# Optimization experiments

Measured on AMD Instinct MI355X. Metric: run time of the kernel, lower is better.

The kernel has to match this reference:

```python
import jax, jax.numpy as jnp
import numpy as np

EPS = 1e-7  # tf.keras.backend.epsilon()
ROUTING = 3
C, L = 32, 32

def squash(s):
    # 'Dynamic routing between capsules' squash: (|s|^2/(1+|s|^2)) * s/|s|
    n = jnp.linalg.norm(s, axis=-1, keepdims=True)
    return (n ** 2 / (1 + n ** 2) / (n + EPS)) * s

def setup_inputs() -> dict:
    key = jax.random.key(0)
    k1, k2 = jax.random.split(key)
    B, H, Wd, iC, iL = 32, 8, 8, 32, 32
    inputs = jax.random.normal(k1, (B, H, Wd, iC, iL), dtype=jnp.float32)
    N = H * Wd * iC  # 2048 input capsules
    # glorot_uniform for W: [N, input_L, C*L]
    limit = float(np.sqrt(6.0 / (iL + C * L)))
    W = jax.random.uniform(k2, (N, iL, C * L), minval=-limit, maxval=limit, dtype=jnp.float32)
    biases = jnp.zeros((C, L), dtype=jnp.float32)  # 'zeros' initializer
    return {"inputs": inputs, "W": W, "biases": biases}

def reference(inputs, W, biases):
    B = inputs.shape[0]
    N, iL = W.shape[0], W.shape[1]
    x = inputs.reshape(B, N, iL)
    # per-capsule prediction: u[b,j,k] = sum_i x[b,j,i] * W[j,i,k]
    u = jnp.einsum('bji,jik->bjk', x, W).reshape(B, N, C, L)
    b = jnp.zeros((B, N, C, 1), dtype=u.dtype)
    v = jnp.zeros((B, C, L), dtype=u.dtype)
    for r in range(ROUTING):
        c = jax.nn.softmax(b, axis=2)                 # coupling coeffs over C
        s = jnp.sum(u * c, axis=1) + biases           # [B,C,L]
        # NOTE: CapsuleAttentionBlock applied here in original (source not
        # provided in this module); treated as identity.
        v = squash(s)                                 # [B,C,L]
        if r < ROUTING - 1:
            b = b + jnp.sum(u * v[:, None, :, :], axis=-1, keepdims=True)
    return v
```

## Files before the change

kernel.cpp:

```cpp
#include <hip/hip_runtime.h>
#include <hip/hip_bf16.h>

#define NB    32
#define NCAP  2048
#define CL    1024
#define ILEN  32

__device__ inline unsigned short f32_to_bf16_rne(float f) {
    unsigned int u = __float_as_uint(f);
    u += 0x7FFFu + ((u >> 16) & 1u);
    return (unsigned short)(u >> 16);
}

__device__ inline void unpack8(uint4 a, float* f) {
    f[0] = __uint_as_float(a.x << 16);
    f[1] = __uint_as_float(a.x & 0xFFFF0000u);
    f[2] = __uint_as_float(a.y << 16);
    f[3] = __uint_as_float(a.y & 0xFFFF0000u);
    f[4] = __uint_as_float(a.z << 16);
    f[5] = __uint_as_float(a.z & 0xFFFF0000u);
    f[6] = __uint_as_float(a.w << 16);
    f[7] = __uint_as_float(a.w & 0xFFFF0000u);
}

__global__ __launch_bounds__(256) void compute_u(const float* __restrict__ x,
                                                 const float* __restrict__ W,
                                                 unsigned short* __restrict__ u) {
    const int j  = blockIdx.x >> 2;
    const int kq = blockIdx.x & 3;
    const int t  = threadIdx.x;

    __shared__ float xs[32 * 32];

    {
        int b  = t >> 3;
        int i4 = (t & 7) << 2;
        float4 v = *(const float4*)(x + ((size_t)b * NCAP + j) * ILEN + i4);
        xs[(i4 + 0) * 32 + b] = v.x;
        xs[(i4 + 1) * 32 + b] = v.y;
        xs[(i4 + 2) * 32 + b] = v.z;
        xs[(i4 + 3) * 32 + b] = v.w;
    }
    __syncthreads();

    const int lane = t & 63;
    const int wv   = t >> 6;

    const float* Wp = W + (size_t)j * (ILEN * CL) + kq * 256 + (lane << 2);

    float acc[8][4];
#pragma unroll
    for (int bb = 0; bb < 8; ++bb)
#pragma unroll
        for (int q = 0; q < 4; ++q) acc[bb][q] = 0.f;

    float4 wbuf[4];
#pragma unroll
    for (int p = 0; p < 4; ++p) wbuf[p] = *(const float4*)(Wp + (size_t)p * CL);

#pragma unroll
    for (int i = 0; i < 32; ++i) {
        float4 w4 = wbuf[i & 3];
        if (i + 4 < 32) wbuf[i & 3] = *(const float4*)(Wp + (size_t)(i + 4) * CL);
        float4 xa = *(const float4*)(xs + i * 32 + wv * 8);
        float4 xb = *(const float4*)(xs + i * 32 + wv * 8 + 4);
        float xv[8] = {xa.x, xa.y, xa.z, xa.w, xb.x, xb.y, xb.z, xb.w};
#pragma unroll
        for (int bb = 0; bb < 8; ++bb) {
            acc[bb][0] += xv[bb] * w4.x;
            acc[bb][1] += xv[bb] * w4.y;
            acc[bb][2] += xv[bb] * w4.z;
            acc[bb][3] += xv[bb] * w4.w;
        }
    }

    const int k = kq * 256 + (lane << 2);
#pragma unroll
    for (int bb = 0; bb < 8; ++bb) {
        int b = wv * 8 + bb;
        ushort4 o;
        o.x = f32_to_bf16_rne(acc[bb][0]);
        o.y = f32_to_bf16_rne(acc[bb][1]);
        o.z = f32_to_bf16_rne(acc[bb][2]);
        o.w = f32_to_bf16_rne(acc[bb][3]);
        *(ushort4*)(u + ((size_t)b * NCAP + j) * CL + k) = o;
    }
}

template<bool HAS_V>
__global__ __launch_bounds__(256) void route_pass(const unsigned short* __restrict__ u,
                                                  const float* __restrict__ vlog,
                                                  float* __restrict__ spart) {
    const int b    = blockIdx.x;
    const int jc   = blockIdx.y;
    const int t    = threadIdx.x;
    const int wv   = t >> 6;
    const int lane = t & 63;
    const int c0   = lane >> 2;
    const int sub  = lane & 3;
    const int e0   = c0 * 32 + sub * 8;

    float vme0[8], vme1[8];
    if (HAS_V) {
        const float* vb = vlog + b * CL;
        *(float4*)(vme0)     = *(const float4*)(vb + e0);
        *(float4*)(vme0 + 4) = *(const float4*)(vb + e0 + 4);
        *(float4*)(vme1)     = *(const float4*)(vb + e0 + 512);
        *(float4*)(vme1 + 4) = *(const float4*)(vb + e0 + 516);
    }

    const int jbase = jc * 64 + wv * 16;
    const unsigned short* ub = u + ((size_t)b * NCAP + jbase) * CL;

    float acc0[8], acc1[8];
#pragma unroll
    for (int e = 0; e < 8; ++e) { acc0[e] = 0.f; acc1[e] = 0.f; }

    uint4 a0 = *(const uint4*)(ub + 0 * CL + e0);
    uint4 g0 = *(const uint4*)(ub + 0 * CL + e0 + 512);
    uint4 a1 = *(const uint4*)(ub + 1 * CL + e0);
    uint4 g1 = *(const uint4*)(ub + 1 * CL + e0 + 512);

    for (int jj = 0; jj < 16; ++jj) {
        int jn = (jj + 2 < 16) ? (jj + 2) : 15;
        uint4 a2 = *(const uint4*)(ub + (size_t)jn * CL + e0);
        uint4 g2 = *(const uint4*)(ub + (size_t)jn * CL + e0 + 512);

        float uf0[8], uf1[8];
        unpack8(a0, uf0);
        unpack8(g0, uf1);

        float cw0, cw1;
        if (HAS_V) {
            float p0 = 0.f, p1 = 0.f;
#pragma unroll
            for (int e = 0; e < 8; ++e) { p0 += uf0[e] * vme0[e]; p1 += uf1[e] * vme1[e]; }
            p0 += __shfl_xor(p0, 1); p0 += __shfl_xor(p0, 2);
            p1 += __shfl_xor(p1, 1); p1 += __shfl_xor(p1, 2);
            float m = fmaxf(p0, p1);
            m = fmaxf(m, __shfl_xor(m, 4));
            m = fmaxf(m, __shfl_xor(m, 8));
            m = fmaxf(m, __shfl_xor(m, 16));
            m = fmaxf(m, __shfl_xor(m, 32));
            float ex0 = __expf(p0 - m);
            float ex1 = __expf(p1 - m);
            float ssum = ex0 + ex1;
            ssum += __shfl_xor(ssum, 4);
            ssum += __shfl_xor(ssum, 8);
            ssum += __shfl_xor(ssum, 16);
            ssum += __shfl_xor(ssum, 32);
            float inv = __builtin_amdgcn_rcpf(ssum);
            cw0 = ex0 * inv;
            cw1 = ex1 * inv;
        } else {
            cw0 = 0.03125f;
            cw1 = 0.03125f;
        }
#pragma unroll
        for (int e = 0; e < 8; ++e) {
            acc0[e] += cw0 * uf0[e];
            acc1[e] += cw1 * uf1[e];
        }
        a0 = a1; g0 = g1; a1 = a2; g1 = g2;
    }

    __shared__ float red[4][1024];
    *(float4*)(&red[wv][e0])       = *(float4*)(acc0);
    *(float4*)(&red[wv][e0 + 4])   = *(float4*)(acc0 + 4);
    *(float4*)(&red[wv][e0 + 512]) = *(float4*)(acc1);
    *(float4*)(&red[wv][e0 + 516]) = *(float4*)(acc1 + 4);
    __syncthreads();

    const int o = t * 4;
    float4 r0 = *(float4*)(&red[0][o]);
    float4 r1 = *(float4*)(&red[1][o]);
    float4 r2 = *(float4*)(&red[2][o]);
    float4 r3 = *(float4*)(&red[3][o]);
    float4 r;
    r.x = (r0.x + r1.x) + (r2.x + r3.x);
    r.y = (r0.y + r1.y) + (r2.y + r3.y);
    r.z = (r0.z + r1.z) + (r2.z + r3.z);
    r.w = (r0.w + r1.w) + (r2.w + r3.w);
    *(float4*)(spart + ((size_t)b * 32 + jc) * CL + o) = r;
}

__global__ __launch_bounds__(256) void squash_kernel(const float* __restrict__ spart,
                                                     const float* __restrict__ biases,
                                                     float* __restrict__ vout,
                                                     float* __restrict__ vlog_out,
                                                     const float* __restrict__ vprev) {
    const int b = blockIdx.x;
    const int t = threadIdx.x;

    float4 sv = make_float4(0.f, 0.f, 0.f, 0.f);
#pragma unroll
    for (int p = 0; p < 32; ++p) {
        float4 q = *(const float4*)(spart + ((size_t)b * 32 + p) * CL + t * 4);
        sv.x += q.x; sv.y += q.y; sv.z += q.z; sv.w += q.w;
    }
    float4 bi = *(const float4*)(biases + t * 4);
    sv.x += bi.x; sv.y += bi.y; sv.z += bi.z; sv.w += bi.w;

    float n2 = sv.x * sv.x + sv.y * sv.y + sv.z * sv.z + sv.w * sv.w;
    n2 += __shfl_xor(n2, 1);
    n2 += __shfl_xor(n2, 2);
    n2 += __shfl_xor(n2, 4);

    float n = sqrtf(n2);
    float f = n2 / ((1.f + n2) * (n + 1e-7f));

    float4 v;
    v.x = f * sv.x; v.y = f * sv.y; v.z = f * sv.z; v.w = f * sv.w;
    *(float4*)(vout + b * CL + t * 4) = v;

    if (vlog_out != nullptr) {
        float4 a = make_float4(0.f, 0.f, 0.f, 0.f);
        if (vprev != nullptr) a = *(const float4*)(vprev + b * CL + t * 4);
        float4 o;
        o.x = v.x + a.x; o.y = v.y + a.y; o.z = v.z + a.z; o.w = v.w + a.w;
        *(float4*)(vlog_out + b * CL + t * 4) = o;
    }
}

extern "C" void kernel_launch(void* const* d_in, const int* in_sizes, int n_in,
                              void* d_out, int out_size, void* d_ws, size_t ws_size,
                              hipStream_t stream) {
    const float* x      = (const float*)d_in[0];
    const float* W      = (const float*)d_in[1];
    const float* biases = (const float*)d_in[2];
    float* out = (float*)d_out;

    unsigned short* u = (unsigned short*)d_ws;
    float* fb    = (float*)((char*)d_ws + (size_t)NB * NCAP * CL * 2);
    float* spart = fb;
    float* v0    = spart + 1048576;
    float* vl2   = v0 + 32768;
    float* vdmp  = vl2 + 32768;

    compute_u<<<NCAP * 4, 256, 0, stream>>>(x, W, u);

    dim3 rg(NB, 32);
    route_pass<false><<<rg, 256, 0, stream>>>(u, nullptr, spart);
    squash_kernel<<<NB, 256, 0, stream>>>(spart, biases, v0, nullptr, nullptr);
    route_pass<true><<<rg, 256, 0, stream>>>(u, v0, spart);
    squash_kernel<<<NB, 256, 0, stream>>>(spart, biases, vdmp, vl2, v0);
    route_pass<true><<<rg, 256, 0, stream>>>(u, vl2, spart);
    squash_kernel<<<NB, 256, 0, stream>>>(spart, biases, out, nullptr, nullptr);
}
```

Before: 468.5 us.

## Fuse first routing pass into prediction kernel via per-tile partial sums

The prediction kernel now handles 16 capsules per block and also accumulates the uniform-coupling first-iteration sum in registers, writing per-tile partial sums. This removes the first full `route_pass` read of the bf16 prediction tensor. The price is a grid that shrinks from 8192 to 512 blocks, which lowers latency hiding on the W stream. It also adds a 16 MB partial buffer that a 32-block squash kernel must reduce over 128 partials.

```diff
diff --git a/kernel.cpp b/kernel.cpp
--- a/kernel.cpp
+++ b/kernel.cpp
@@ -5,6 +5,7 @@
 #define NCAP  2048
 #define CL    1024
 #define ILEN  32
+#define JT    16
 
 __device__ inline unsigned short f32_to_bf16_rne(float f) {
     unsigned int u = __float_as_uint(f);
@@ -23,67 +24,98 @@
     f[7] = __uint_as_float(a.w & 0xFFFF0000u);
 }
 
-__global__ __launch_bounds__(256) void compute_u(const float* __restrict__ x,
-                                                 const float* __restrict__ W,
-                                                 unsigned short* __restrict__ u) {
-    const int j  = blockIdx.x >> 2;
+__global__ __launch_bounds__(256) void compute_u_fused(const float* __restrict__ x,
+                                                       const float* __restrict__ W,
+                                                       unsigned short* __restrict__ u,
+                                                       float* __restrict__ s0part) {
+    const int jt = blockIdx.x >> 2;
     const int kq = blockIdx.x & 3;
+    const int j0 = jt * JT;
     const int t  = threadIdx.x;
 
-    __shared__ float xs[32 * 32];
+    __shared__ float xs[JT][32][32];
 
     {
-        int b  = t >> 3;
-        int i4 = (t & 7) << 2;
-        float4 v = *(const float4*)(x + ((size_t)b * NCAP + j) * ILEN + i4);
-        xs[(i4 + 0) * 32 + b] = v.x;
-        xs[(i4 + 1) * 32 + b] = v.y;
-        xs[(i4 + 2) * 32 + b] = v.z;
-        xs[(i4 + 3) * 32 + b] = v.w;
+        const int b  = t >> 3;
+        const int i4 = (t & 7) << 2;
+#pragma unroll
+        for (int jj = 0; jj < JT; ++jj) {
+            float4 v = *(const float4*)(x + ((size_t)b * NCAP + j0 + jj) * ILEN + i4);
+            xs[jj][i4 + 0][b] = v.x;
+            xs[jj][i4 + 1][b] = v.y;
+            xs[jj][i4 + 2][b] = v.z;
+            xs[jj][i4 + 3][b] = v.w;
+        }
     }
     __syncthreads();
 
     const int lane = t & 63;
     const int wv   = t >> 6;
 
-    const float* Wp = W + (size_t)j * (ILEN * CL) + kq * 256 + (lane << 2);
-
-    float acc[8][4];
+    const float* Wp = W + (size_t)j0 * (ILEN * CL) + kq * 256 + (lane << 2);
+    const int k = kq * 256 + (lane << 2);
+
+    float s0[8][4];
 #pragma unroll
     for (int bb = 0; bb < 8; ++bb)
 #pragma unroll
-        for (int q = 0; q < 4; ++q) acc[bb][q] = 0.f;
-
-    float4 wbuf[4];
-#pragma unroll
-    for (int p = 0; p < 4; ++p) wbuf[p] = *(const float4*)(Wp + (size_t)p * CL);
-
-#pragma unroll
-    for (int i = 0; i < 32; ++i) {
-        float4 w4 = wbuf[i & 3];
-        if (i + 4 < 32) wbuf[i & 3] = *(const float4*)(Wp + (size_t)(i + 4) * CL);
-        float4 xa = *(const float4*)(xs + i * 32 + wv * 8);
-        float4 xb = *(const float4*)(xs + i * 32 + wv * 8 + 4);
-        float xv[8] = {xa.x, xa.y, xa.z, xa.w, xb.x, xb.y, xb.z, xb.w};
+        for (int q = 0; q < 4; ++q) s0[bb][q] = 0.f;
+
+    float4 ring[4];
+#pragma unroll
+    for (int p = 0; p < 4; ++p) ring[p] = *(const float4*)(Wp + (size_t)p * CL);
+
+    for (int jj = 0; jj < JT; ++jj) {
+        float acc[8][4];
+#pragma unroll
+        for (int bb = 0; bb < 8; ++bb)
+#pragma unroll
+            for (int q = 0; q < 4; ++q) acc[bb][q] = 0.f;
+
+#pragma unroll
+        for (int i = 0; i < 32; ++i) {
+            float4 w4 = ring[i & 3];
+            int rn = jj * 32 + i + 4;
+            if (rn > JT * 32 - 1) rn = JT * 32 - 1;
+            ring[i & 3] = *(const float4*)(Wp + (size_t)rn * CL);
+
+            float4 xa = *(const float4*)(&xs[jj][i][wv * 8]);
+            float4 xb = *(const float4*)(&xs[jj][i][wv * 8 + 4]);
+            float xv[8] = {xa.x, xa.y, xa.z, xa.w, xb.x, xb.y, xb.z, xb.w};
+#pragma unroll
+            for (int bb = 0; bb < 8; ++bb) {
+                acc[bb][0] += xv[bb] * w4.x;
+                acc[bb][1] += xv[bb] * w4.y;
+                acc[bb][2] += xv[bb] * w4.z;
+                acc[bb][3] += xv[bb] * w4.w;
+            }
+        }
+
 #pragma unroll
         for (int bb = 0; bb < 8; ++bb) {
-            acc[bb][0] += xv[bb] * w4.x;
-            acc[bb][1] += xv[bb] * w4.y;
-            acc[bb][2] += xv[bb] * w4.z;
-            acc[bb][3] += xv[bb] * w4.w;
-        }
-    }
-
-    const int k = kq * 256 + (lane << 2);
+            const int b = wv * 8 + bb;
+            s0[bb][0] += acc[bb][0];
+            s0[bb][1] += acc[bb][1];
+            s0[bb][2] += acc[bb][2];
+            s0[bb][3] += acc[bb][3];
+            ushort4 o;
+            o.x = f32_to_bf16_rne(acc[bb][0]);
+            o.y = f32_to_bf16_rne(acc[bb][1]);
+            o.z = f32_to_bf16_rne(acc[bb][2]);
+            o.w = f32_to_bf16_rne(acc[bb][3]);
+            *(ushort4*)(u + ((size_t)b * NCAP + j0 + jj) * CL + k) = o;
+        }
+    }
+
 #pragma unroll
     for (int bb = 0; bb < 8; ++bb) {
-        int b = wv * 8 + bb;
-        ushort4 o;
-        o.x = f32_to_bf16_rne(acc[bb][0]);
-        o.y = f32_to_bf16_rne(acc[bb][1]);
-        o.z = f32_to_bf16_rne(acc[bb][2]);
-        o.w = f32_to_bf16_rne(acc[bb][3]);
-        *(ushort4*)(u + ((size_t)b * NCAP + j) * CL + k) = o;
+        const int b = wv * 8 + bb;
+        float4 o;
+        o.x = s0[bb][0] * 0.03125f;
+        o.y = s0[bb][1] * 0.03125f;
+        o.z = s0[bb][2] * 0.03125f;
+        o.w = s0[bb][3] * 0.03125f;
+        *(float4*)(s0part + ((size_t)b * 128 + jt) * CL + k) = o;
     }
 }
 
@@ -184,6 +216,7 @@
     *(float4*)(spart + ((size_t)b * 32 + jc) * CL + o) = r;
 }
 
+template<int P>
 __global__ __launch_bounds__(256) void squash_kernel(const float* __restrict__ spart,
                                                      const float* __restrict__ biases,
                                                      float* __restrict__ vout,
@@ -193,9 +226,9 @@
     const int t = threadIdx.x;
 
     float4 sv = make_float4(0.f, 0.f, 0.f, 0.f);
-#pragma unroll
-    for (int p = 0; p < 32; ++p) {
-        float4 q = *(const float4*)(spart + ((size_t)b * 32 + p) * CL + t * 4);
+#pragma unroll 8
+    for (int p = 0; p < P; ++p) {
+        float4 q = *(const float4*)(spart + ((size_t)b * P + p) * CL + t * 4);
         sv.x += q.x; sv.y += q.y; sv.z += q.z; sv.w += q.w;
     }
     float4 bi = *(const float4*)(biases + t * 4);
@@ -231,19 +264,18 @@
     float* out = (float*)d_out;
 
     unsigned short* u = (unsigned short*)d_ws;
-    float* fb    = (float*)((char*)d_ws + (size_t)NB * NCAP * CL * 2);
-    float* spart = fb;
-    float* v0    = spart + 1048576;
-    float* vl2   = v0 + 32768;
-    float* vdmp  = vl2 + 32768;
-
-    compute_u<<<NCAP * 4, 256, 0, stream>>>(x, W, u);
-
+    float* fb     = (float*)((char*)d_ws + (size_t)NB * NCAP * CL * 2);
+    float* s0part = fb;
+    float* spart  = s0part + 4194304;
+    float* v0     = spart + 1048576;
+    float* vl2    = v0 + 32768;
+    float* vdmp   = vl2 + 32768;
+
+    compute_u_fused<<<512, 256, 0, stream>>>(x, W, u, s0part);
+    squash_kernel<128><<<NB, 256, 0, stream>>>(s0part, biases, v0, nullptr, nullptr);
     dim3 rg(NB, 32);
-    route_pass<false><<<rg, 256, 0, stream>>>(u, nullptr, spart);
-    squash_kernel<<<NB, 256, 0, stream>>>(spart, biases, v0, nullptr, nullptr);
     route_pass<true><<<rg, 256, 0, stream>>>(u, v0, spart);
-    squash_kernel<<<NB, 256, 0, stream>>>(spart, biases, vdmp, vl2, v0);
+    squash_kernel<32><<<NB, 256, 0, stream>>>(spart, biases, vdmp, vl2, v0);
     route_pass<true><<<rg, 256, 0, stream>>>(u, vl2, spart);
-    squash_kernel<<<NB, 256, 0, stream>>>(spart, biases, out, nullptr, nullptr);
-}
+    squash_kernel<32><<<NB, 256, 0, stream>>>(spart, biases, out, nullptr, nullptr);
+}
```

Measured after the change: 599.5 us. 28.0% more time.
